# Performance work log

Hardware: AMD Instinct MI355X
Metric: run time of the kernel (lower is better)

## Reference

```python
import math
import jax, jax.numpy as jnp
import numpy as np

D_MODEL = 896
N_HEADS = 14
D_HEAD = D_MODEL // N_HEADS  # 64
ROPE_BASE = 10000.0
LN_EPS = 1e-5
B, N = 8, 1024


def setup_inputs() -> dict:
    key = jax.random.key(0)
    ks = jax.random.split(key, 12)
    s = 1.0 / math.sqrt(D_MODEL)
    return {
        "node_features": jax.random.normal(ks[0], (B, N, D_MODEL), jnp.float32),
        "adj": jax.random.uniform(ks[1], (N, N), jnp.float32),
        "wind_dirs": jax.random.uniform(ks[2], (B, N), jnp.float32),
        "bearings": jax.random.uniform(ks[3], (N, N), jnp.float32),
        "Wq": jax.random.normal(ks[4], (D_MODEL, D_MODEL), jnp.float32) * s,
        "Wk": jax.random.normal(ks[5], (D_MODEL, D_MODEL), jnp.float32) * s,
        "Wv": jax.random.normal(ks[6], (D_MODEL, D_MODEL), jnp.float32) * s,
        "Wo": jax.random.normal(ks[7], (D_MODEL, D_MODEL), jnp.float32) * s,
        "ln_g": jnp.ones((D_MODEL,), jnp.float32),
        "ln_b": jnp.zeros((D_MODEL,), jnp.float32),
        "wind_w": jax.random.normal(ks[8], (2, N_HEADS), jnp.float32) * (1.0 / math.sqrt(2.0)),
        "wind_b": jnp.zeros((N_HEADS,), jnp.float32),
    }


def _layernorm(x, g, b):
    mu = jnp.mean(x, axis=-1, keepdims=True)
    var = jnp.var(x, axis=-1, keepdims=True)
    return (x - mu) * jax.lax.rsqrt(var + LN_EPS) * g + b


def _apply_rotary(x, cos_h, sin_h):
    # x: (B,H,N,d_head); cos_h/sin_h: (N, d_head//2)
    d_half = x.shape[-1] // 2
    x1, x2 = x[..., :d_half], x[..., d_half:]
    return jnp.concatenate([x1 * cos_h - x2 * sin_h, x2 * cos_h + x1 * sin_h], axis=-1)


def reference(node_features, adj, wind_dirs, bearings, Wq, Wk, Wv, Wo, ln_g, ln_b, wind_w, wind_b):
    Bb, Nn, D = node_features.shape
    residual = node_features
    x = _layernorm(node_features, ln_g, ln_b)

    def proj(W):
        return (x @ W).reshape(Bb, Nn, N_HEADS, D_HEAD).transpose(0, 2, 1, 3)  # (B,H,N,dh)

    Q, K, V = proj(Wq), proj(Wk), proj(Wv)

    # RoPE: cos/sin halves (first d_half entries of the duplicated freq table)
    inv_freq = 1.0 / (ROPE_BASE ** (jnp.arange(0, D_HEAD, 2, dtype=jnp.float32) / D_HEAD))
    freqs = jnp.arange(Nn, dtype=jnp.float32)[:, None] * inv_freq[None, :]  # (N, dh/2)
    cos_h, sin_h = jnp.cos(freqs), jnp.sin(freqs)
    Q = _apply_rotary(Q, cos_h, sin_h)
    K = _apply_rotary(K, cos_h, sin_h)

    attn = jnp.einsum("bhqd,bhkd->bhqk", Q, K) / math.sqrt(D_HEAD)
    adj_mask = (adj > 0)[None, None, :, :]
    attn = jnp.where(adj_mask, attn, -1e30)

    # wind-direction dynamic edge bias
    reverse_bearings = (bearings.T + 180.0) % 360.0  # (N,N)
    alignment = jnp.cos(jnp.deg2rad(wind_dirs[:, :, None] - reverse_bearings[None]))  # (B,N,N)
    dist_feat = jnp.broadcast_to(adj[None], (Bb, Nn, Nn))
    edge_features = jnp.stack([alignment, dist_feat], axis=-1)  # (B,N,N,2)
    wind_bias = jnp.tanh(edge_features @ wind_w + wind_b)  # (B,N,N,H)
    attn = attn + wind_bias.transpose(0, 3, 1, 2)  # (B,H,N,N)

    attn = jax.nn.softmax(attn, axis=-1)  # dropout is identity in eval
    out = jnp.einsum("bhqk,bhkd->bhqd", attn, V)
    out = out.transpose(0, 2, 1, 3).reshape(Bb, Nn, D) @ Wo
    return residual + out
```

## Files before the change

### kernel.cpp

```cpp
#include <hip/hip_runtime.h>
#include <hip/hip_bf16.h>
#include <math.h>

#define B_ 8
#define N_ 1024
#define H_ 14
#define DH_ 64
#define D_ 896
#define M_ (B_*N_)
#define DQKV_ 2688

#define TWO_LOG2E_ 2.8853900817779268f
#define BIAS_C_   (-15.869645449778597f)
#define QSCALE_     0.18033688011112043f

typedef __attribute__((ext_vector_type(8))) short bf16x8;
typedef __attribute__((ext_vector_type(4))) short bf16x4;
typedef __attribute__((ext_vector_type(4))) float f32x4;
typedef __attribute__((ext_vector_type(4))) unsigned u32x4;

__device__ __forceinline__ float bf2f(short s){
  unsigned u = ((unsigned)(unsigned short)s) << 16;
  union { unsigned u; float f; } c; c.u = u; return c.f;
}
__device__ __forceinline__ short f2bf(float f){
  union { float f; unsigned u; } c; c.f = f;
  unsigned u = c.u;
  unsigned r = (u + 0x7FFFu + ((u >> 16) & 1u)) >> 16;
  return (short)(unsigned short)r;
}
__device__ __forceinline__ float asf(unsigned u){
  union { unsigned u; float f; } c; c.u = u; return c.f;
}
__device__ __forceinline__ unsigned cvt_pk_bf16(float lo, float hi){
  unsigned r;
  asm("v_cvt_pk_bf16_f32 %0, %1, %2" : "=v"(r) : "v"(lo), "v"(hi));
  return r;
}

#define BAR_LDS() do { asm volatile("s_waitcnt lgkmcnt(0)" ::: "memory"); \
                       __builtin_amdgcn_s_barrier(); } while (0)

__global__ __launch_bounds__(256) void ln_kernel(const float* __restrict__ x,
                                                 const float* __restrict__ g,
                                                 const float* __restrict__ bb,
                                                 short* __restrict__ y)
{
  int row = blockIdx.x;
  const float* xr = x + (size_t)row * D_;
  float s = 0.f, s2 = 0.f;
  for (int i = threadIdx.x; i < D_; i += 256){
    float v = xr[i]; s += v; s2 = fmaf(v, v, s2);
  }
  #pragma unroll
  for (int off = 32; off > 0; off >>= 1){
    s  += __shfl_down(s,  off, 64);
    s2 += __shfl_down(s2, off, 64);
  }
  __shared__ float rs_[4], rs2_[4];
  int wv = threadIdx.x >> 6;
  if ((threadIdx.x & 63) == 0){ rs_[wv] = s; rs2_[wv] = s2; }
  __syncthreads();
  float ts  = rs_[0] + rs_[1] + rs_[2] + rs_[3];
  float ts2 = rs2_[0] + rs2_[1] + rs2_[2] + rs2_[3];
  float mu  = ts * (1.f / D_);
  float var = ts2 * (1.f / D_) - mu * mu;
  float rstd = rsqrtf(var + 1e-5f);
  short* yr = y + (size_t)row * D_;
  for (int i = threadIdx.x; i < D_; i += 256){
    yr[i] = f2bf((xr[i] - mu) * rstd * g[i] + bb[i]);
  }
}

__global__ __launch_bounds__(256) void transpose_kernel(
    const float* __restrict__ Wq, const float* __restrict__ Wk,
    const float* __restrict__ Wv, const float* __restrict__ Wo,
    short* __restrict__ WqkvT, short* __restrict__ WoT)
{
  __shared__ short t[64][72];
  int z = blockIdx.z;
  const float* W = (z == 0) ? Wq : (z == 1) ? Wk : (z == 2) ? Wv : Wo;
  int kb = blockIdx.x * 64, nb = blockIdx.y * 64;
  int c0 = (threadIdx.x & 7) * 8;
  int r0 = threadIdx.x >> 3;
  #pragma unroll
  for (int rr = 0; rr < 64; rr += 32){
    const float* src = &W[(size_t)(kb + r0 + rr) * D_ + nb + c0];
    float4 a = *(const float4*)src;
    float4 b = *(const float4*)(src + 4);
    short* dstl = &t[r0 + rr][c0];
    dstl[0] = f2bf(a.x); dstl[1] = f2bf(a.y); dstl[2] = f2bf(a.z); dstl[3] = f2bf(a.w);
    dstl[4] = f2bf(b.x); dstl[5] = f2bf(b.y); dstl[6] = f2bf(b.z); dstl[7] = f2bf(b.w);
  }
  __syncthreads();
  short* dst = (z < 3) ? (WqkvT + (size_t)(z * D_) * D_) : WoT;
  #pragma unroll
  for (int rr = 0; rr < 64; rr += 32){
    int n = nb + r0 + rr;
    bf16x8 v;
    #pragma unroll
    for (int j = 0; j < 8; j++) v[j] = t[c0 + j][r0 + rr];
    *(bf16x8*)&dst[(size_t)n * D_ + kb + c0] = v;
  }
}

__global__ __launch_bounds__(256) void prep_kernel(
    const float* __restrict__ adj, const float* __restrict__ brg,
    const float* __restrict__ wdir,
    unsigned* __restrict__ csb, short* __restrict__ adjT,
    short* __restrict__ alignT, int do_align)
{
  int kt = blockIdx.x, qt = blockIdx.y;
  __shared__ short tt[64][72];
  __shared__ float cA_[8][64], sA_[8][64];

  if (do_align){
    for (int idx = threadIdx.x; idx < 8 * 64; idx += 256){
      int b = idx >> 6, q = idx & 63;
      float A = wdir[(size_t)b * N_ + qt * 64 + q] * 0.017453292519943295f;
      float s, c; __sincosf(A, &s, &c);
      sA_[b][q] = s; cA_[b][q] = c;
    }
  }

  int r  = threadIdx.x >> 2;
  int c0 = (threadIdx.x & 3) * 16;

  {
    int q = qt * 64 + r;
    const float* ap = adj + (size_t)q * N_ + kt * 64 + c0;
    #pragma unroll
    for (int i = 0; i < 16; i += 4){
      float4 av = *(const float4*)(ap + i);
      tt[r][c0 + i]     = f2bf(av.x);
      tt[r][c0 + i + 1] = f2bf(av.y);
      tt[r][c0 + i + 2] = f2bf(av.z);
      tt[r][c0 + i + 3] = f2bf(av.w);
    }
  }
  __syncthreads();

  int k = kt * 64 + r;
  float cB[16], sB[16];
  {
    const float* bp = brg + (size_t)k * N_ + qt * 64 + c0;
    #pragma unroll
    for (int i = 0; i < 16; i += 4){
      float4 bv = *(const float4*)(bp + i);
      float b4[4] = { bv.x, bv.y, bv.z, bv.w };
      #pragma unroll
      for (int j = 0; j < 4; j++){
        float Br = (b4[j] + 180.f) * 0.017453292519943295f;
        __sincosf(Br, &sB[i + j], &cB[i + j]);
      }
    }
  }

  if (do_align){
    #pragma unroll
    for (int b = 0; b < 8; b++){
      unsigned w8[8];
      #pragma unroll
      for (int p = 0; p < 8; p++){
        int q0i = c0 + 2 * p, q1i = q0i + 1;
        float a0 = fmaf(cA_[b][q0i], cB[2 * p],     sA_[b][q0i] * sB[2 * p]);
        float a1 = fmaf(cA_[b][q1i], cB[2 * p + 1], sA_[b][q1i] * sB[2 * p + 1]);
        w8[p] = cvt_pk_bf16(a0, a1);
      }
      short* dst = alignT + ((size_t)b * N_ + k) * N_ + qt * 64 + c0;
      *(uint4*)dst       = make_uint4(w8[0], w8[1], w8[2], w8[3]);
      *(uint4*)(dst + 8) = make_uint4(w8[4], w8[5], w8[6], w8[7]);
    }
  } else {
    unsigned* cp = csb + (size_t)k * N_ + qt * 64 + c0;
    #pragma unroll
    for (int i = 0; i < 16; i += 4){
      unsigned o[4];
      #pragma unroll
      for (int j = 0; j < 4; j++)
        o[j] = ((unsigned)(unsigned short)f2bf(cB[i + j])) |
               (((unsigned)(unsigned short)f2bf(sB[i + j])) << 16);
      *(uint4*)(cp + i) = make_uint4(o[0], o[1], o[2], o[3]);
    }
  }

  {
    short* op = adjT + (size_t)k * N_ + qt * 64 + c0;
    bf16x8 v0, v1;
    #pragma unroll
    for (int j = 0; j < 8; j++){ v0[j] = tt[c0 + j][r]; v1[j] = tt[c0 + 8 + j][r]; }
    *(bf16x8*)op = v0;
    *(bf16x8*)(op + 8) = v1;
  }
}

__global__ __launch_bounds__(256) void gemm_bt(const short* __restrict__ A,
                                               const short* __restrict__ Bt,
                                               short* __restrict__ C,
                                               float* __restrict__ Cf,
                                               const float* __restrict__ residf,
                                               int N, int rope)
{
  const int K = D_;
  __shared__ short As[128 * 32];
  __shared__ short Bs[128 * 32];
  int tid  = threadIdx.x;
  int wave = tid >> 6;
  int lane = tid & 63;
  int quad = lane >> 4;
  int l16  = lane & 15;
  int wr = wave >> 1, wc = wave & 1;
  int m0 = blockIdx.x * 128;
  int n0 = blockIdx.y * 128;

  f32x4 acc[4][4];
  #pragma unroll
  for (int i = 0; i < 4; i++)
    #pragma unroll
    for (int j = 0; j < 4; j++)
      acc[i][j] = (f32x4){0.f, 0.f, 0.f, 0.f};

  for (int k0 = 0; k0 < K; k0 += 32){
    __syncthreads();
    #pragma unroll
    for (int it = 0; it < 2; ++it){
      int c   = tid + it * 256;
      int row = c >> 2;
      int cc  = c & 3;
      const short* ga = A  + (size_t)(m0 + row) * K + k0 + cc * 8;
      const short* gb = Bt + (size_t)(n0 + row) * K + k0 + cc * 8;
      short* la = As + (size_t)(wave * 64 + it * 256) * 8;
      short* lb = Bs + (size_t)(wave * 64 + it * 256) * 8;
      __builtin_amdgcn_global_load_lds((const __attribute__((address_space(1))) void*)ga,
                                       (__attribute__((address_space(3))) void*)la, 16, 0, 0);
      __builtin_amdgcn_global_load_lds((const __attribute__((address_space(1))) void*)gb,
                                       (__attribute__((address_space(3))) void*)lb, 16, 0, 0);
    }
    __syncthreads();

    bf16x8 af[4], bfr[4];
    #pragma unroll
    for (int i = 0; i < 4; i++)
      af[i] = *(const bf16x8*)(As + (size_t)(wr * 64 + i * 16 + l16) * 32 + quad * 8);
    #pragma unroll
    for (int j = 0; j < 4; j++)
      bfr[j] = *(const bf16x8*)(Bs + (size_t)(wc * 64 + j * 16 + l16) * 32 + quad * 8);
    #pragma unroll
    for (int i = 0; i < 4; i++)
      #pragma unroll
      for (int j = 0; j < 4; j++)
        acc[i][j] = __builtin_amdgcn_mfma_f32_16x16x32_bf16(af[i], bfr[j], acc[i][j], 0, 0, 0);
  }

  if (rope){
    int cb  = n0 + wc * 64;
    int mat = cb / D_;
    if (mat < 2){
      float scale = (mat == 0) ? QSCALE_ : 1.0f;
      float invf0 = exp2f(-0.4152410118609203f * (float)l16);
      float invf1 = invf0 * 0.01f;
      #pragma unroll
      for (int i = 0; i < 4; i++){
        #pragma unroll
        for (int rr = 0; rr < 4; rr++){
          int r = m0 + wr * 64 + i * 16 + quad * 4 + rr;
          float nseq = (float)(r & (N_ - 1));
          float s0, c0v, s1, c1v;
          __sincosf(nseq * invf0, &s0, &c0v);
          __sincosf(nseq * invf1, &s1, &c1v);
          float x1 = acc[i][0][rr], x2 = acc[i][2][rr];
          acc[i][0][rr] = (x1 * c0v - x2 * s0) * scale;
          acc[i][2][rr] = (x2 * c0v + x1 * s0) * scale;
          x1 = acc[i][1][rr]; x2 = acc[i][3][rr];
          acc[i][1][rr] = (x1 * c1v - x2 * s1) * scale;
          acc[i][3][rr] = (x2 * c1v + x1 * s1) * scale;
        }
      }
    }
  }

  #pragma unroll
  for (int i = 0; i < 4; i++){
    #pragma unroll
    for (int rr = 0; rr < 4; rr++){
      int r = m0 + wr * 64 + i * 16 + quad * 4 + rr;
      size_t rowoff = (size_t)r * N;
      #pragma unroll
      for (int j = 0; j < 4; j++){
        int cidx = n0 + wc * 64 + j * 16 + l16;
        float v = acc[i][j][rr];
        if (Cf){
          Cf[rowoff + cidx] = v + residf[rowoff + cidx];
        } else {
          C[rowoff + cidx] = f2bf(v);
        }
      }
    }
  }
}

template<int PRE>
__global__ __launch_bounds__(256, 4) void attn_kernel(
    const short* __restrict__ QKV,
    const unsigned* __restrict__ csb,
    const short* __restrict__ adjT,
    const short* __restrict__ alignT,
    const float* __restrict__ wind_dirs,
    const float* __restrict__ wind_w,
    const float* __restrict__ wind_b,
    short* __restrict__ outb)
{
  __shared__ short K_s[64 * 72];
  __shared__ short V_t[64 * 76];
  __shared__ short P_s[64 * 76];

  int bid = blockIdx.x;
  int qt  = bid / 112;
  int rem = bid - qt * 112;
  int hh  = rem >> 3;
  int b   = rem & 7;
  int q0  = qt * 64;
  int kt0 = qt;

  int t    = threadIdx.x;
  int w    = t >> 6;
  int lane = t & 63;
  int quad = lane >> 4;
  int l16  = lane & 15;

  const short* qp = QKV + ((size_t)(b * N_) + q0 + w * 16 + l16) * DQKV_ + hh * DH_;
  bf16x8 qf0 = *(const bf16x8*)(qp + quad * 8);
  bf16x8 qf1 = *(const bf16x8*)(qp + 32 + quad * 8);

  float cA[4], sA[4];
  if (!PRE){
    #pragma unroll
    for (int rr = 0; rr < 4; rr++){
      float wd = wind_dirs[(size_t)b * N_ + q0 + w * 16 + quad * 4 + rr];
      float A  = wd * 0.017453292519943295f;
      sA[rr] = __sinf(A);
      cA[rr] = __cosf(A);
    }
  }
  float w0m = wind_w[hh]      * TWO_LOG2E_;
  float w1m = wind_w[H_ + hh] * TWO_LOG2E_;
  float wbm = wind_b[hh]      * TWO_LOG2E_;

  float l[4] = {0.f, 0.f, 0.f, 0.f};
  f32x4 O[4];
  #pragma unroll
  for (int dc = 0; dc < 4; dc++) O[dc] = (f32x4){0.f, 0.f, 0.f, 0.f};

  int kr   = t >> 2, kc16 = (t & 3) * 16;
  int vk4  = (t >> 4) * 4, vd4 = (t & 15) * 4;
  const short* kg0 = QKV + ((size_t)(b * N_) + kr)  * DQKV_ + D_     + hh * DH_ + kc16;
  const short* vg0 = QKV + ((size_t)(b * N_) + vk4) * DQKV_ + 2 * D_ + hh * DH_ + vd4;

  int k0f = kt0 * 64;
  bf16x8 pk0 = *(const bf16x8*)(kg0 + (size_t)k0f * DQKV_);
  bf16x8 pk1 = *(const bf16x8*)(kg0 + (size_t)k0f * DQKV_ + 8);
  bf16x4 pv0 = *(const bf16x4*)(vg0 + (size_t)(k0f + 0) * DQKV_);
  bf16x4 pv1 = *(const bf16x4*)(vg0 + (size_t)(k0f + 1) * DQKV_);
  bf16x4 pv2 = *(const bf16x4*)(vg0 + (size_t)(k0f + 2) * DQKV_);
  bf16x4 pv3 = *(const bf16x4*)(vg0 + (size_t)(k0f + 3) * DQKV_);

  size_t bias_q = (size_t)(q0 + w * 16 + quad * 4);
  u32x4 cs4a[4]; bf16x4 al4a[4]; bf16x4 av4a[4];
  #pragma unroll
  for (int jc = 0; jc < 4; jc++){
    size_t off = (size_t)(k0f + jc * 16 + l16) * N_ + bias_q;
    if (PRE) al4a[jc] = *(const bf16x4*)(alignT + (size_t)b * N_ * N_ + off);
    else     cs4a[jc] = *(const u32x4*)(csb + off);
    av4a[jc] = *(const bf16x4*)(adjT + off);
  }

  for (int it = 0; it < 16; ++it){
    int ktn = (it + 1 + kt0) & 15;
    int kn  = ktn * 64;

    BAR_LDS();
    *(bf16x8*)(K_s + kr * 72 + kc16)     = pk0;
    *(bf16x8*)(K_s + kr * 72 + kc16 + 8) = pk1;
    #pragma unroll
    for (int j = 0; j < 4; j++){
      unsigned lo = ((unsigned)(unsigned short)pv0[j]) |
                    (((unsigned)(unsigned short)pv1[j]) << 16);
      unsigned hi = ((unsigned)(unsigned short)pv2[j]) |
                    (((unsigned)(unsigned short)pv3[j]) << 16);
      *(uint2*)(V_t + (vd4 + j) * 76 + vk4) = make_uint2(lo, hi);
    }
    BAR_LDS();

    pk0 = *(const bf16x8*)(kg0 + (size_t)kn * DQKV_);
    pk1 = *(const bf16x8*)(kg0 + (size_t)kn * DQKV_ + 8);
    pv0 = *(const bf16x4*)(vg0 + (size_t)(kn + 0) * DQKV_);
    pv1 = *(const bf16x4*)(vg0 + (size_t)(kn + 1) * DQKV_);
    pv2 = *(const bf16x4*)(vg0 + (size_t)(kn + 2) * DQKV_);
    pv3 = *(const bf16x4*)(vg0 + (size_t)(kn + 3) * DQKV_);

    f32x4 S[4];
    __builtin_amdgcn_s_setprio(1);
    #pragma unroll
    for (int jc = 0; jc < 4; jc++){
      S[jc] = (f32x4){0.f, 0.f, 0.f, 0.f};
      bf16x8 kf0 = *(const bf16x8*)(K_s + (jc * 16 + l16) * 72 + quad * 8);
      bf16x8 kf1 = *(const bf16x8*)(K_s + (jc * 16 + l16) * 72 + 32 + quad * 8);
      S[jc] = __builtin_amdgcn_mfma_f32_16x16x32_bf16(qf0, kf0, S[jc], 0, 0, 0);
      S[jc] = __builtin_amdgcn_mfma_f32_16x16x32_bf16(qf1, kf1, S[jc], 0, 0, 0);
    }
    __builtin_amdgcn_s_setprio(0);

    #pragma unroll
    for (int kc = 0; kc < 2; kc++){
      #pragma unroll
      for (int jc = kc * 2; jc < kc * 2 + 2; jc++){
        float ev[4];
        #pragma unroll
        for (int rr = 0; rr < 4; rr++){
          float av = bf2f(av4a[jc][rr]);
          float align;
          if (PRE){
            align = bf2f(al4a[jc][rr]);
          } else {
            unsigned u = cs4a[jc][rr];
            float cB = asf(u << 16);
            float sB = asf(u & 0xffff0000u);
            align = cA[rr] * cB + sA[rr] * sB;
          }
          float z2 = fmaf(align, w0m, fmaf(av, w1m, wbm));
          float e2 = __builtin_amdgcn_exp2f(z2);
          float rc = __builtin_amdgcn_rcpf(e2 + 1.f);
          float bias2 = fmaf(-TWO_LOG2E_, rc, BIAS_C_);
          float sv = (av > 0.f ? S[jc][rr] : -1e30f) + bias2;
          float e = __builtin_amdgcn_exp2f(sv);
          l[rr] += e;
          ev[rr] = e;
        }
        unsigned pk01 = cvt_pk_bf16(ev[0], ev[1]);
        unsigned pk23 = cvt_pk_bf16(ev[2], ev[3]);
        short* pb = P_s + (w * 16 + quad * 4) * 76 + jc * 16 + l16;
        pb[0]   = (short)pk01;
        pb[76]  = (short)(pk01 >> 16);
        pb[152] = (short)pk23;
        pb[228] = (short)(pk23 >> 16);
      }

      __builtin_amdgcn_s_setprio(1);
      {
        const short* pp = P_s + (w * 16 + l16) * 76 + kc * 32 + quad * 8;
        bf16x4 p0 = *(const bf16x4*)pp;
        bf16x4 p1 = *(const bf16x4*)(pp + 4);
        bf16x8 pf = { p0[0], p0[1], p0[2], p0[3], p1[0], p1[1], p1[2], p1[3] };
        #pragma unroll
        for (int dc = 0; dc < 4; dc++){
          const short* vp = V_t + (dc * 16 + l16) * 76 + kc * 32 + quad * 8;
          bf16x4 u0 = *(const bf16x4*)vp;
          bf16x4 u1 = *(const bf16x4*)(vp + 4);
          bf16x8 vf = { u0[0], u0[1], u0[2], u0[3], u1[0], u1[1], u1[2], u1[3] };
          O[dc] = __builtin_amdgcn_mfma_f32_16x16x32_bf16(pf, vf, O[dc], 0, 0, 0);
        }
      }
      __builtin_amdgcn_s_setprio(0);

      #pragma unroll
      for (int jc = kc * 2; jc < kc * 2 + 2; jc++){
        size_t off = (size_t)(kn + jc * 16 + l16) * N_ + bias_q;
        if (PRE) al4a[jc] = *(const bf16x4*)(alignT + (size_t)b * N_ * N_ + off);
        else     cs4a[jc] = *(const u32x4*)(csb + off);
        av4a[jc] = *(const bf16x4*)(adjT + off);
      }
    }
  }

  float rl[4];
  #pragma unroll
  for (int rr = 0; rr < 4; rr++){
    float rs = l[rr];
    rs += __shfl_xor(rs, 1);
    rs += __shfl_xor(rs, 2);
    rs += __shfl_xor(rs, 4);
    rs += __shfl_xor(rs, 8);
    rl[rr] = 1.f / rs;
  }
  short* op = outb + ((size_t)(b * N_) + q0 + w * 16) * D_ + hh * DH_;
  #pragma unroll
  for (int rr = 0; rr < 4; rr++)
    #pragma unroll
    for (int dc = 0; dc < 4; dc++)
      op[(size_t)(quad * 4 + rr) * D_ + dc * 16 + l16] = f2bf(O[dc][rr] * rl[rr]);
}

extern "C" void kernel_launch(void* const* d_in, const int* in_sizes, int n_in,
                              void* d_out, int out_size, void* d_ws, size_t ws_size,
                              hipStream_t stream)
{
  const float* nf   = (const float*)d_in[0];
  const float* adj  = (const float*)d_in[1];
  const float* wdir = (const float*)d_in[2];
  const float* brg  = (const float*)d_in[3];
  const float* Wq   = (const float*)d_in[4];
  const float* Wk   = (const float*)d_in[5];
  const float* Wv   = (const float*)d_in[6];
  const float* Wo   = (const float*)d_in[7];
  const float* lng  = (const float*)d_in[8];
  const float* lnb  = (const float*)d_in[9];
  const float* ww   = (const float*)d_in[10];
  const float* wbb  = (const float*)d_in[11];
  float* out = (float*)d_out;

  short* base = (short*)d_ws;
  size_t sh = 0;
  short* xln   = base + sh;  sh += (size_t)M_ * D_;
  short* WqkvT = base + sh;  sh += (size_t)DQKV_ * D_;
  short* WoT   = base + sh;  sh += (size_t)D_ * D_;
  short* QKV   = base + sh;  sh += (size_t)M_ * DQKV_;
  unsigned* csb = (unsigned*)(base + sh); sh += (size_t)N_ * N_ * 2;
  short* adjT  = base + sh;  sh += (size_t)N_ * N_;
  short* alignT = base + sh; sh += (size_t)B_ * N_ * N_;
  size_t need_pre = sh * sizeof(short);
  bool pre = (ws_size >= need_pre);

  ln_kernel<<<M_, 256, 0, stream>>>(nf, lng, lnb, xln);
  transpose_kernel<<<dim3(14, 14, 4), 256, 0, stream>>>(Wq, Wk, Wv, Wo, WqkvT, WoT);
  prep_kernel<<<dim3(16, 16), 256, 0, stream>>>(adj, brg, wdir, csb, adjT, alignT, pre ? 1 : 0);
  gemm_bt<<<dim3(M_ / 128, DQKV_ / 128), 256, 0, stream>>>(xln, WqkvT, QKV, nullptr, nullptr, DQKV_, 1);
  if (pre)
    attn_kernel<1><<<B_ * H_ * 16, 256, 0, stream>>>(QKV, csb, adjT, alignT, wdir, ww, wbb, xln);
  else
    attn_kernel<0><<<B_ * H_ * 16, 256, 0, stream>>>(QKV, csb, adjT, alignT, wdir, ww, wbb, xln);
  gemm_bt<<<dim3(M_ / 128, D_ / 128), 256, 0, stream>>>(xln, WoT, nullptr, out, nf, D_, 0);
}
```

Before: 371.3 us.

## Load K and pre-transposed V fragments directly from global, dropping LDS staging

```diff
diff --git a/kernel.cpp b/kernel.cpp
--- a/kernel.cpp
+++ b/kernel.cpp
@@ -37,9 +37,6 @@
   asm("v_cvt_pk_bf16_f32 %0, %1, %2" : "=v"(r) : "v"(lo), "v"(hi));
   return r;
 }
-
-#define BAR_LDS() do { asm volatile("s_waitcnt lgkmcnt(0)" ::: "memory"); \
-                       __builtin_amdgcn_s_barrier(); } while (0)
 
 __global__ __launch_bounds__(256) void ln_kernel(const float* __restrict__ x,
                                                  const float* __restrict__ g,
@@ -102,6 +99,27 @@
     for (int j = 0; j < 8; j++) v[j] = t[c0 + j][r0 + rr];
     *(bf16x8*)&dst[(size_t)n * D_ + kb + c0] = v;
   }
+}
+
+__global__ __launch_bounds__(256) void vt_kernel(const short* __restrict__ QKV,
+                                                 short* __restrict__ VT)
+{
+  __shared__ short tt[64][72];
+  int kt = blockIdx.x;
+  int bh = blockIdx.y;
+  int b  = bh / H_, hh = bh - b * H_;
+  int r  = threadIdx.x >> 2;
+  int c0 = (threadIdx.x & 3) * 16;
+  const short* src = QKV + ((size_t)(b * N_) + kt * 64 + r) * DQKV_ + 2 * D_ + hh * DH_ + c0;
+  *(bf16x8*)&tt[r][c0]     = *(const bf16x8*)src;
+  *(bf16x8*)&tt[r][c0 + 8] = *(const bf16x8*)(src + 8);
+  __syncthreads();
+  short* dst = VT + ((size_t)bh * DH_ + r) * N_ + kt * 64 + c0;
+  bf16x8 v0, v1;
+  #pragma unroll
+  for (int j = 0; j < 8; j++){ v0[j] = tt[c0 + j][r]; v1[j] = tt[c0 + 8 + j][r]; }
+  *(bf16x8*)dst       = v0;
+  *(bf16x8*)(dst + 8) = v1;
 }
 
 __global__ __launch_bounds__(256) void prep_kernel(
@@ -302,6 +320,7 @@
 template<int PRE>
 __global__ __launch_bounds__(256, 4) void attn_kernel(
     const short* __restrict__ QKV,
+    const short* __restrict__ VT,
     const unsigned* __restrict__ csb,
     const short* __restrict__ adjT,
     const short* __restrict__ alignT,
@@ -310,8 +329,6 @@
     const float* __restrict__ wind_b,
     short* __restrict__ outb)
 {
-  __shared__ short K_s[64 * 72];
-  __shared__ short V_t[64 * 76];
   __shared__ short P_s[64 * 76];
 
   int bid = blockIdx.x;
@@ -351,62 +368,43 @@
   #pragma unroll
   for (int dc = 0; dc < 4; dc++) O[dc] = (f32x4){0.f, 0.f, 0.f, 0.f};
 
-  int kr   = t >> 2, kc16 = (t & 3) * 16;
-  int vk4  = (t >> 4) * 4, vd4 = (t & 15) * 4;
-  const short* kg0 = QKV + ((size_t)(b * N_) + kr)  * DQKV_ + D_     + hh * DH_ + kc16;
-  const short* vg0 = QKV + ((size_t)(b * N_) + vk4) * DQKV_ + 2 * D_ + hh * DH_ + vd4;
-
-  int k0f = kt0 * 64;
-  bf16x8 pk0 = *(const bf16x8*)(kg0 + (size_t)k0f * DQKV_);
-  bf16x8 pk1 = *(const bf16x8*)(kg0 + (size_t)k0f * DQKV_ + 8);
-  bf16x4 pv0 = *(const bf16x4*)(vg0 + (size_t)(k0f + 0) * DQKV_);
-  bf16x4 pv1 = *(const bf16x4*)(vg0 + (size_t)(k0f + 1) * DQKV_);
-  bf16x4 pv2 = *(const bf16x4*)(vg0 + (size_t)(k0f + 2) * DQKV_);
-  bf16x4 pv3 = *(const bf16x4*)(vg0 + (size_t)(k0f + 3) * DQKV_);
-
+  const short* kbase = QKV + (size_t)(b * N_) * DQKV_ + D_ + hh * DH_ + quad * 8;
+  const short* vbase = VT + ((size_t)(b * H_ + hh) * DH_) * N_;
   size_t bias_q = (size_t)(q0 + w * 16 + quad * 4);
-  u32x4 cs4a[4]; bf16x4 al4a[4]; bf16x4 av4a[4];
-  #pragma unroll
-  for (int jc = 0; jc < 4; jc++){
-    size_t off = (size_t)(k0f + jc * 16 + l16) * N_ + bias_q;
-    if (PRE) al4a[jc] = *(const bf16x4*)(alignT + (size_t)b * N_ * N_ + off);
-    else     cs4a[jc] = *(const u32x4*)(csb + off);
-    av4a[jc] = *(const bf16x4*)(adjT + off);
-  }
 
   for (int it = 0; it < 16; ++it){
-    int ktn = (it + 1 + kt0) & 15;
-    int kn  = ktn * 64;
-
-    BAR_LDS();
-    *(bf16x8*)(K_s + kr * 72 + kc16)     = pk0;
-    *(bf16x8*)(K_s + kr * 72 + kc16 + 8) = pk1;
-    #pragma unroll
-    for (int j = 0; j < 4; j++){
-      unsigned lo = ((unsigned)(unsigned short)pv0[j]) |
-                    (((unsigned)(unsigned short)pv1[j]) << 16);
-      unsigned hi = ((unsigned)(unsigned short)pv2[j]) |
-                    (((unsigned)(unsigned short)pv3[j]) << 16);
-      *(uint2*)(V_t + (vd4 + j) * 76 + vk4) = make_uint2(lo, hi);
-    }
-    BAR_LDS();
-
-    pk0 = *(const bf16x8*)(kg0 + (size_t)kn * DQKV_);
-    pk1 = *(const bf16x8*)(kg0 + (size_t)kn * DQKV_ + 8);
-    pv0 = *(const bf16x4*)(vg0 + (size_t)(kn + 0) * DQKV_);
-    pv1 = *(const bf16x4*)(vg0 + (size_t)(kn + 1) * DQKV_);
-    pv2 = *(const bf16x4*)(vg0 + (size_t)(kn + 2) * DQKV_);
-    pv3 = *(const bf16x4*)(vg0 + (size_t)(kn + 3) * DQKV_);
+    int k0 = ((it + kt0) & 15) * 64;
+
+    bf16x8 kf[4][2];
+    #pragma unroll
+    for (int jc = 0; jc < 4; jc++){
+      const short* kp = kbase + (size_t)(k0 + jc * 16 + l16) * DQKV_;
+      kf[jc][0] = *(const bf16x8*)kp;
+      kf[jc][1] = *(const bf16x8*)(kp + 32);
+    }
+    bf16x8 vf[2][4];
+    #pragma unroll
+    for (int kc = 0; kc < 2; kc++)
+      #pragma unroll
+      for (int dc = 0; dc < 4; dc++)
+        vf[kc][dc] = *(const bf16x8*)(vbase + (size_t)(dc * 16 + l16) * N_ +
+                                      k0 + kc * 32 + quad * 8);
+    u32x4 cs4a[4]; bf16x4 al4a[4]; bf16x4 av4a[4];
+    #pragma unroll
+    for (int jc = 0; jc < 4; jc++){
+      size_t off = (size_t)(k0 + jc * 16 + l16) * N_ + bias_q;
+      if (PRE) al4a[jc] = *(const bf16x4*)(alignT + (size_t)b * N_ * N_ + off);
+      else     cs4a[jc] = *(const u32x4*)(csb + off);
+      av4a[jc] = *(const bf16x4*)(adjT + off);
+    }
 
     f32x4 S[4];
     __builtin_amdgcn_s_setprio(1);
     #pragma unroll
     for (int jc = 0; jc < 4; jc++){
       S[jc] = (f32x4){0.f, 0.f, 0.f, 0.f};
-      bf16x8 kf0 = *(const bf16x8*)(K_s + (jc * 16 + l16) * 72 + quad * 8);
-      bf16x8 kf1 = *(const bf16x8*)(K_s + (jc * 16 + l16) * 72 + 32 + quad * 8);
-      S[jc] = __builtin_amdgcn_mfma_f32_16x16x32_bf16(qf0, kf0, S[jc], 0, 0, 0);
-      S[jc] = __builtin_amdgcn_mfma_f32_16x16x32_bf16(qf1, kf1, S[jc], 0, 0, 0);
+      S[jc] = __builtin_amdgcn_mfma_f32_16x16x32_bf16(qf0, kf[jc][0], S[jc], 0, 0, 0);
+      S[jc] = __builtin_amdgcn_mfma_f32_16x16x32_bf16(qf1, kf[jc][1], S[jc], 0, 0, 0);
     }
     __builtin_amdgcn_s_setprio(0);
 
@@ -452,23 +450,10 @@
         bf16x4 p1 = *(const bf16x4*)(pp + 4);
         bf16x8 pf = { p0[0], p0[1], p0[2], p0[3], p1[0], p1[1], p1[2], p1[3] };
         #pragma unroll
-        for (int dc = 0; dc < 4; dc++){
-          const short* vp = V_t + (dc * 16 + l16) * 76 + kc * 32 + quad * 8;
-          bf16x4 u0 = *(const bf16x4*)vp;
-          bf16x4 u1 = *(const bf16x4*)(vp + 4);
-          bf16x8 vf = { u0[0], u0[1], u0[2], u0[3], u1[0], u1[1], u1[2], u1[3] };
-          O[dc] = __builtin_amdgcn_mfma_f32_16x16x32_bf16(pf, vf, O[dc], 0, 0, 0);
-        }
+        for (int dc = 0; dc < 4; dc++)
+          O[dc] = __builtin_amdgcn_mfma_f32_16x16x32_bf16(pf, vf[kc][dc], O[dc], 0, 0, 0);
       }
       __builtin_amdgcn_s_setprio(0);
-
-      #pragma unroll
-      for (int jc = kc * 2; jc < kc * 2 + 2; jc++){
-        size_t off = (size_t)(kn + jc * 16 + l16) * N_ + bias_q;
-        if (PRE) al4a[jc] = *(const bf16x4*)(alignT + (size_t)b * N_ * N_ + off);
-        else     cs4a[jc] = *(const u32x4*)(csb + off);
-        av4a[jc] = *(const bf16x4*)(adjT + off);
-      }
     }
   }
 
@@ -514,6 +499,7 @@
   short* WqkvT = base + sh;  sh += (size_t)DQKV_ * D_;
   short* WoT   = base + sh;  sh += (size_t)D_ * D_;
   short* QKV   = base + sh;  sh += (size_t)M_ * DQKV_;
+  short* VT    = base + sh;  sh += (size_t)B_ * H_ * DH_ * N_;
   unsigned* csb = (unsigned*)(base + sh); sh += (size_t)N_ * N_ * 2;
   short* adjT  = base + sh;  sh += (size_t)N_ * N_;
   short* alignT = base + sh; sh += (size_t)B_ * N_ * N_;
@@ -524,9 +510,10 @@
   transpose_kernel<<<dim3(14, 14, 4), 256, 0, stream>>>(Wq, Wk, Wv, Wo, WqkvT, WoT);
   prep_kernel<<<dim3(16, 16), 256, 0, stream>>>(adj, brg, wdir, csb, adjT, alignT, pre ? 1 : 0);
   gemm_bt<<<dim3(M_ / 128, DQKV_ / 128), 256, 0, stream>>>(xln, WqkvT, QKV, nullptr, nullptr, DQKV_, 1);
+  vt_kernel<<<dim3(16, 112), 256, 0, stream>>>(QKV, VT);
   if (pre)
-    attn_kernel<1><<<B_ * H_ * 16, 256, 0, stream>>>(QKV, csb, adjT, alignT, wdir, ww, wbb, xln);
+    attn_kernel<1><<<B_ * H_ * 16, 256, 0, stream>>>(QKV, VT, csb, adjT, alignT, wdir, ww, wbb, xln);
   else
-    attn_kernel<0><<<B_ * H_ * 16, 256, 0, stream>>>(QKV, csb, adjT, alignT, wdir, ww, wbb, xln);
+    attn_kernel<0><<<B_ * H_ * 16, 256, 0, stream>>>(QKV, VT, csb, adjT, alignT, wdir, ww, wbb, xln);
   gemm_bt<<<dim3(M_ / 128, D_ / 128), 256, 0, stream>>>(xln, WoT, nullptr, out, nf, D_, 0);
 }
```

Result: slower. 592.4 us (+59.5%).
